# Optimization experiments

Hardware: AMD Instinct MI355X
Metric: run time of the kernel (lower is better)

The kernel has to match this reference:

```python
import jax, jax.numpy as jnp
import numpy as np

N_NODES = 50000
N_EDGES = 800000
IN_CH = 64
HID = 128


def setup_inputs() -> dict:
    key = jax.random.key(0)
    ks = jax.random.split(key, 10)
    x = jax.random.normal(ks[0], (N_NODES, IN_CH), dtype=jnp.float32)
    edge_index = jax.random.randint(ks[1], (2, N_EDGES), 0, N_NODES, dtype=jnp.int64)
    def lin(k, fan_in, fan_out):
        bound = 1.0 / np.sqrt(fan_in)
        kw, kb = jax.random.split(k)
        W = jax.random.uniform(kw, (fan_in, fan_out), minval=-bound, maxval=bound, dtype=jnp.float32)
        b = jax.random.uniform(kb, (fan_out,), minval=-bound, maxval=bound, dtype=jnp.float32)
        return W, b
    W1a, b1a = lin(ks[2], 2 * IN_CH, HID)
    W1b, b1b = lin(ks[3], HID, HID)
    W2a, b2a = lin(ks[4], 2 * HID, HID)
    W2b, b2b = lin(ks[5], HID, HID)
    return {"x": x, "edge_index": edge_index,
            "W1a": W1a, "b1a": b1a, "W1b": W1b, "b1b": b1b,
            "W2a": W2a, "b2a": b2a, "W2b": W2b, "b2b": b2b}


def _edge_conv(x, src, dst, Wa, ba, Wb, bb):
    # PyG EdgeConv: message = MLP([x_i, x_j - x_i]), aggr = max at target i (dst)
    xi = x[dst]                                   # [E, C] target feats
    xj = x[src]                                   # [E, C] source feats
    m = jnp.concatenate([xi, xj - xi], axis=-1)   # [E, 2C]
    m = jax.nn.relu(m @ Wa + ba) @ Wb + bb        # [E, H]
    agg = jax.ops.segment_max(m, dst, num_segments=N_NODES)
    # nodes with no incoming edge -> 0 (torch_scatter fill value)
    return jnp.where(jnp.isfinite(agg), agg, 0.0)


def reference(x, edge_index, W1a, b1a, W1b, b1b, W2a, b2a, W2b, b2b):
    src = edge_index[0]
    dst = edge_index[1]
    h = _edge_conv(x, src, dst, W1a, b1a, W1b, b1b)
    h = jax.nn.relu(h)
    h = _edge_conv(h, src, dst, W2a, b2a, W2b, b2b)
    return h
```

## Files before the change

kernel.cpp:

```cpp
#include <hip/hip_runtime.h>
#include <stdint.h>

#define N_NODES 50000
#define N_EDGES 800000
#define HID 128
#define NWG_E (N_EDGES / 128)
#define XQ (NWG_E / 8)
#define XR (NWG_E % 8)
#define SCAN_B 196

#define ENC_NEG_INF 0x007FFFFFu

typedef short short8 __attribute__((ext_vector_type(8)));
typedef float f32x4 __attribute__((ext_vector_type(4)));

__device__ __forceinline__ unsigned enc_f32(float f) {
    unsigned u = __float_as_uint(f);
    return (u & 0x80000000u) ? ~u : (u | 0x80000000u);
}
__device__ __forceinline__ float dec_f32(unsigned e) {
    unsigned u = (e & 0x80000000u) ? (e & 0x7FFFFFFFu) : ~e;
    return __uint_as_float(u);
}
__device__ __forceinline__ unsigned short f2bf(float f) {
    unsigned u = __float_as_uint(f);
    unsigned r = (u + 0x7fffu + ((u >> 16) & 1u)) >> 16;
    return (unsigned short)r;
}
__device__ __forceinline__ float bf2f(unsigned short h) {
    return __uint_as_float(((unsigned)h) << 16);
}
__device__ __forceinline__ float wcat_val(const float* __restrict__ W, int K, int k, int n) {
    return (n < 128) ? (W[k * 128 + n] - W[(k + K) * 128 + n]) : W[(k + K) * 128 + (n - 128)];
}

__global__ __launch_bounds__(256) void setup(
        const float* __restrict__ W1a, const float* __restrict__ W1b,
        const float* __restrict__ W2a, const float* __restrict__ W2b,
        unsigned short* __restrict__ Wg1, unsigned short* __restrict__ Wg2,
        unsigned short* __restrict__ WCg1, unsigned short* __restrict__ WCg2,
        unsigned* __restrict__ AGG1, unsigned* __restrict__ OUT,
        unsigned* __restrict__ count) {
    int bid = blockIdx.x, tid = threadIdx.x;
    const int NH = N_NODES * HID;

    if (bid < 128) {
        const float* Wb = (bid < 64) ? W1b : W2b;
        unsigned short* Wg = (bid < 64) ? Wg1 : Wg2;
        int idx = (bid & 63) * 256 + tid;
        int j = idx & 7, l = (idx >> 3) & 63, t = idx >> 9;
        int h = t >> 4, kt = (t >> 2) & 3, ntl = t & 3;
        int nt = 4 * h + ntl;
        int k = 32 * kt + 8 * (l >> 4) + j;
        int n = 16 * nt + (l & 15);
        Wg[idx] = f2bf(Wb[k * 128 + n]);
    } else if (bid < 192) {
        int idx = (bid - 128) * 256 + tid;
        int j = idx & 7, l = (idx >> 3) & 63, nt = (idx >> 9) & 15, kt = idx >> 13;
        int k = 32 * kt + 8 * (l >> 4) + j;
        int n = 16 * nt + (l & 15);
        float v = wcat_val(W1a, 64, k, n);
        unsigned short hi = f2bf(v);
        WCg1[idx] = hi;
        WCg1[64 * 256 + idx] = f2bf(v - bf2f(hi));
    } else if (bid < 320) {
        int idx = (bid - 192) * 256 + tid;
        int j = idx & 7, l = (idx >> 3) & 63, nt = (idx >> 9) & 15, kt = idx >> 13;
        int k = 32 * kt + 8 * (l >> 4) + j;
        int n = 16 * nt + (l & 15);
        float v = wcat_val(W2a, 128, k, n);
        unsigned short hi = f2bf(v);
        WCg2[idx] = hi;
        WCg2[128 * 256 + idx] = f2bf(v - bf2f(hi));
    }

    int total = 2 * NH + N_NODES;
    for (int i = bid * 256 + tid; i < total; i += gridDim.x * 256) {
        if (i < NH) AGG1[i] = ENC_NEG_INF;
        else if (i < 2 * NH) OUT[i - NH] = ENC_NEG_INF;
        else count[i - 2 * NH] = 0u;
    }
}

__global__ void out_decode(unsigned* __restrict__ p, const float* __restrict__ bias, int n) {
    int i = blockIdx.x * blockDim.x + threadIdx.x;
    int stride = gridDim.x * blockDim.x;
    for (; i < n; i += stride) {
        unsigned e = p[i];
        float f = (e == ENC_NEG_INF) ? 0.0f : dec_f32(e) + bias[i & 127];
        ((float*)p)[i] = f;
    }
}


__global__ void hist_dst(const int* __restrict__ dst, unsigned* __restrict__ count) {
    int i = blockIdx.x * blockDim.x + threadIdx.x;
    if (i < N_EDGES) atomicAdd(&count[dst[i]], 1u);
}

__global__ __launch_bounds__(256) void scan_p1(const unsigned* __restrict__ count,
                                               unsigned* __restrict__ bsum) {
    __shared__ unsigned s[256];
    int t = threadIdx.x;
    int i = blockIdx.x * 256 + t;
    s[t] = (i < N_NODES) ? count[i] : 0u;
    __syncthreads();
    for (int off = 128; off > 0; off >>= 1) {
        if (t < off) s[t] += s[t + off];
        __syncthreads();
    }
    if (t == 0) bsum[blockIdx.x] = s[0];
}

__global__ __launch_bounds__(256) void scan_p2(unsigned* __restrict__ bsum) {
    __shared__ unsigned s[256];
    int t = threadIdx.x;
    unsigned v = (t < SCAN_B) ? bsum[t] : 0u;
    s[t] = v;
    __syncthreads();
    for (int off = 1; off < 256; off <<= 1) {
        unsigned x = (t >= off) ? s[t - off] : 0u;
        __syncthreads();
        s[t] += x;
        __syncthreads();
    }
    if (t < SCAN_B) bsum[t] = s[t] - v;
}

__global__ __launch_bounds__(256) void scan_p3(const unsigned* __restrict__ count,
                                               const unsigned* __restrict__ bsum,
                                               unsigned* __restrict__ cursor) {
    __shared__ unsigned s[256];
    int t = threadIdx.x;
    int i = blockIdx.x * 256 + t;
    unsigned v = (i < N_NODES) ? count[i] : 0u;
    s[t] = v;
    __syncthreads();
    for (int off = 1; off < 256; off <<= 1) {
        unsigned x = (t >= off) ? s[t - off] : 0u;
        __syncthreads();
        s[t] += x;
        __syncthreads();
    }
    if (i < N_NODES) cursor[i] = bsum[blockIdx.x] + s[t] - v;
}

__global__ void scatter_edges(const int* __restrict__ src, const int* __restrict__ dst,
                              unsigned* __restrict__ cursor,
                              int* __restrict__ ssrc, int* __restrict__ sdst) {
    int i = blockIdx.x * blockDim.x + threadIdx.x;
    if (i < N_EDGES) {
        int d = dst[i];
        unsigned p = atomicAdd(&cursor[d], 1u);
        ssrc[p] = src[i];
        sdst[p] = d;
    }
}

template<int DEC, int KT>
__global__ __launch_bounds__(256, 2) void gemm_uv_mfma(
        const void* __restrict__ A_,
        const unsigned short* __restrict__ Wg,
        const float* __restrict__ bprev,
        const float* __restrict__ bu,
        unsigned short* __restrict__ C,
        int M) {
    __shared__ char lds[KT * 8192];
    const int K = 32 * KT;
    int tid = threadIdx.x;
    int bx = blockIdx.x, by = blockIdx.y;
    int r0 = bx * 128;
    int w = tid >> 6, l = tid & 63;
    int q = l >> 4, m = l & 15;

    short8 ahi[2][KT];
#pragma unroll
    for (int mt = 0; mt < 2; ++mt) {
        int row = r0 + 32 * w + 16 * mt + m;
        bool ok = row < M;
#pragma unroll
        for (int kt = 0; kt < KT; ++kt) {
            float av[8] = {0.f, 0.f, 0.f, 0.f, 0.f, 0.f, 0.f, 0.f};
            if (ok) {
                if (DEC) {
                    const unsigned* Ar = (const unsigned*)A_ + (size_t)row * K + 32 * kt + 8 * q;
                    uint4 x0 = *(const uint4*)Ar;
                    uint4 x1 = *(const uint4*)(Ar + 4);
                    float4 g0 = *(const float4*)&bprev[32 * kt + 8 * q];
                    float4 g1 = *(const float4*)&bprev[32 * kt + 8 * q + 4];
                    av[0] = fmaxf(dec_f32(x0.x) + g0.x, 0.f);
                    av[1] = fmaxf(dec_f32(x0.y) + g0.y, 0.f);
                    av[2] = fmaxf(dec_f32(x0.z) + g0.z, 0.f);
                    av[3] = fmaxf(dec_f32(x0.w) + g0.w, 0.f);
                    av[4] = fmaxf(dec_f32(x1.x) + g1.x, 0.f);
                    av[5] = fmaxf(dec_f32(x1.y) + g1.y, 0.f);
                    av[6] = fmaxf(dec_f32(x1.z) + g1.z, 0.f);
                    av[7] = fmaxf(dec_f32(x1.w) + g1.w, 0.f);
                } else {
                    const float* Ar = (const float*)A_ + (size_t)row * K + 32 * kt + 8 * q;
                    float4 f0 = *(const float4*)Ar;
                    float4 f1 = *(const float4*)(Ar + 4);
                    av[0] = f0.x; av[1] = f0.y; av[2] = f0.z; av[3] = f0.w;
                    av[4] = f1.x; av[5] = f1.y; av[6] = f1.z; av[7] = f1.w;
                }
            }
            short8 hi;
#pragma unroll
            for (int j = 0; j < 8; ++j) hi[j] = (short)f2bf(av[j]);
            ahi[mt][kt] = hi;
        }
    }

    f32x4 acc[2][8];
#pragma unroll
    for (int mt = 0; mt < 2; ++mt)
#pragma unroll
        for (int nt = 0; nt < 8; ++nt)
            acc[mt][nt] = (f32x4){0.f, 0.f, 0.f, 0.f};

    const short8* bfr = (const short8*)lds;

#pragma unroll
    for (int pl = 0; pl < 2; ++pl) {
        if (pl) __syncthreads();
        {
            const float4* s4 = (const float4*)Wg + (size_t)pl * (K * 32);
            float4* d4 = (float4*)lds;
#pragma unroll
            for (int it = 0; it < 2 * KT; ++it) {
                int f = 256 * it + tid;
                int tl = f >> 6, fin = f & 63;
                int tg = (tl >> 3) * 16 + 8 * by + (tl & 7);
                d4[f] = s4[tg * 64 + fin];
            }
        }
        __syncthreads();
#pragma unroll
        for (int nt = 0; nt < 8; ++nt)
#pragma unroll
            for (int kt = 0; kt < KT; ++kt) {
                short8 b = bfr[(kt * 8 + nt) * 64 + l];
                acc[0][nt] = __builtin_amdgcn_mfma_f32_16x16x32_bf16(ahi[0][kt], b, acc[0][nt], 0, 0, 0);
                acc[1][nt] = __builtin_amdgcn_mfma_f32_16x16x32_bf16(ahi[1][kt], b, acc[1][nt], 0, 0, 0);
            }
    }

#pragma unroll
    for (int nt = 0; nt < 8; ++nt) {
        float bias = (by == 0) ? bu[16 * nt + m] : 0.f;
#pragma unroll
        for (int mt = 0; mt < 2; ++mt) {
            int rowb = r0 + 32 * w + 16 * mt + 4 * q;
#pragma unroll
            for (int r = 0; r < 4; ++r) {
                int row = rowb + r;
                if (row < M)
                    C[(size_t)row * 256 + 128 * by + 16 * nt + m] = f2bf(acc[mt][nt][r] + bias);
            }
        }
    }
}

__global__ __launch_bounds__(256, 4) void edge_mlp_mfma(
        const unsigned short* __restrict__ UV,
        const unsigned short* __restrict__ Wg,
        const int* __restrict__ ssrc,
        const int* __restrict__ sdst,
        unsigned* __restrict__ AGG) {
    __shared__ char lds[17408];
    __shared__ int sdst_s[128];
    int tid = threadIdx.x;
    int orig = blockIdx.x;
    int xcd = orig & 7, ii = orig >> 3;
    int wg = (xcd < XR) ? xcd * (XQ + 1) + ii : XR * (XQ + 1) + (xcd - XR) * XQ + ii;
    int e0 = wg * 128;
    int w = tid >> 6, l = tid & 63;
    int q = l >> 4, m = l & 15;

    if (tid < 128) sdst_s[tid] = sdst[e0 + tid];

    short8 ahi[2][4];
    {
        int eA = e0 + 32 * w + m;
        int d0 = sdst[eA], s0 = ssrc[eA];
        int d1 = sdst[eA + 16], s1 = ssrc[eA + 16];
        const short8* Ud0 = (const short8*)&UV[(size_t)d0 * 256];
        const short8* Vs0 = (const short8*)&UV[(size_t)s0 * 256 + 128];
        const short8* Ud1 = (const short8*)&UV[(size_t)d1 * 256];
        const short8* Vs1 = (const short8*)&UV[(size_t)s1 * 256 + 128];
        short8 ub[2][4], vb[2][4];
#pragma unroll
        for (int kt = 0; kt < 4; ++kt) {
            ub[0][kt] = Ud0[4 * kt + q];
            vb[0][kt] = Vs0[4 * kt + q];
            ub[1][kt] = Ud1[4 * kt + q];
            vb[1][kt] = Vs1[4 * kt + q];
        }
#pragma unroll
        for (int mt = 0; mt < 2; ++mt)
#pragma unroll
            for (int kt = 0; kt < 4; ++kt) {
                short8 hi;
#pragma unroll
                for (int j = 0; j < 8; ++j) {
                    float t = bf2f((unsigned short)ub[mt][kt][j]) + bf2f((unsigned short)vb[mt][kt][j]);
                    hi[j] = (short)f2bf(fmaxf(t, 0.f));
                }
                ahi[mt][kt] = hi;
            }
    }

    const short8* bfr = (const short8*)lds;
    float* M2 = (float*)lds;
    f32x4 acc[2][4];

#pragma unroll
    for (int h = 0; h < 2; ++h) {
        __syncthreads();
        {
            const float4* s4 = (const float4*)Wg + h * 1024;
            float4* d4 = (float4*)lds;
#pragma unroll
            for (int i = 0; i < 4; ++i) d4[tid + 256 * i] = s4[tid + 256 * i];
        }
        __syncthreads();
#pragma unroll
        for (int mt = 0; mt < 2; ++mt)
#pragma unroll
            for (int ntl = 0; ntl < 4; ++ntl)
                acc[mt][ntl] = (f32x4){0.f, 0.f, 0.f, 0.f};
#pragma unroll
        for (int ntl = 0; ntl < 4; ++ntl)
#pragma unroll
            for (int kt = 0; kt < 4; ++kt) {
                short8 b = bfr[(kt * 4 + ntl) * 64 + l];
                acc[0][ntl] = __builtin_amdgcn_mfma_f32_16x16x32_bf16(ahi[0][kt], b, acc[0][ntl], 0, 0, 0);
                acc[1][ntl] = __builtin_amdgcn_mfma_f32_16x16x32_bf16(ahi[1][kt], b, acc[1][ntl], 0, 0, 0);
            }

#pragma unroll
        for (int cn = 0; cn < 2; ++cn) {
            __syncthreads();
#pragma unroll
            for (int nt2 = 0; nt2 < 2; ++nt2) {
                int ntl = 2 * cn + nt2;
#pragma unroll
                for (int mt = 0; mt < 2; ++mt)
#pragma unroll
                    for (int r = 0; r < 4; ++r)
                        M2[(32 * w + 16 * mt + 4 * q + r) * 34 + 16 * nt2 + m] = acc[mt][ntl][r];
            }
            __syncthreads();
            {
                int c = tid & 31, g = tid >> 5;
                int eb = 16 * g;
                int cur = sdst_s[eb];
                float mx = -3.402823466e38f;
                for (int e2 = eb; e2 < eb + 16; ++e2) {
                    int de = sdst_s[e2];
                    if (de != cur) {
                        atomicMax(&AGG[(size_t)cur * 128 + 64 * h + 32 * cn + c], enc_f32(mx));
                        cur = de;
                        mx = -3.402823466e38f;
                    }
                    mx = fmaxf(mx, M2[e2 * 34 + c]);
                }
                atomicMax(&AGG[(size_t)cur * 128 + 64 * h + 32 * cn + c], enc_f32(mx));
            }
        }
    }
}


extern "C" void kernel_launch(void* const* d_in, const int* in_sizes, int n_in,
                              void* d_out, int out_size, void* d_ws, size_t ws_size,
                              hipStream_t stream) {
    const float* x   = (const float*)d_in[0];
    const int*   ei  = (const int*)d_in[1];
    const float* W1a = (const float*)d_in[2];
    const float* b1a = (const float*)d_in[3];
    const float* W1b = (const float*)d_in[4];
    const float* b1b = (const float*)d_in[5];
    const float* W2a = (const float*)d_in[6];
    const float* b2a = (const float*)d_in[7];
    const float* W2b = (const float*)d_in[8];
    const float* b2b = (const float*)d_in[9];
    const int* src = ei;
    const int* dst = ei + N_EDGES;

    char* ws = (char*)d_ws;
    unsigned short* UV    = (unsigned short*)ws;
    unsigned*       AGG1  = (unsigned*)(ws + 25600000);
    int*            ssrc  = (int*)(ws + 51200000);
    int*            sdst  = (int*)(ws + 54400000);
    unsigned*       count = (unsigned*)(ws + 57600000);
    unsigned*       cursor= (unsigned*)(ws + 57800000);
    unsigned short* Wg1   = (unsigned short*)(ws + 58000000);
    unsigned short* Wg2   = (unsigned short*)(ws + 58065536);
    unsigned short* WCg1  = (unsigned short*)(ws + 58327680);
    unsigned short* WCg2  = (unsigned short*)(ws + 58393216);
    unsigned*       bsum  = (unsigned*)(ws + 58655744);

    const int NH = N_NODES * HID;

    setup<<<2048, 256, 0, stream>>>(W1a, W1b, W2a, W2b, Wg1, Wg2, WCg1, WCg2,
                                    AGG1, (unsigned*)d_out, count);

    hist_dst<<<3125, 256, 0, stream>>>(dst, count);
    scan_p1<<<SCAN_B, 256, 0, stream>>>(count, bsum);
    scan_p2<<<1, 256, 0, stream>>>(bsum);
    scan_p3<<<SCAN_B, 256, 0, stream>>>(count, bsum, cursor);
    scatter_edges<<<3125, 256, 0, stream>>>(src, dst, cursor, ssrc, sdst);

    gemm_uv_mfma<0, 2><<<dim3(391, 2), 256, 0, stream>>>(x, WCg1, nullptr, b1a, UV, N_NODES);
    edge_mlp_mfma<<<NWG_E, 256, 0, stream>>>(UV, Wg1, ssrc, sdst, AGG1);

    gemm_uv_mfma<1, 4><<<dim3(391, 2), 256, 0, stream>>>(AGG1, WCg2, b1b, b2a, UV, N_NODES);
    edge_mlp_mfma<<<NWG_E, 256, 0, stream>>>(UV, Wg2, ssrc, sdst, (unsigned*)d_out);
    out_decode<<<2048, 256, 0, stream>>>((unsigned*)d_out, b2b, NH);
}
```

Measured before the change: 314.9 us.

## Load full weight tile once and use per-wave LDS scratch to drop block barriers

The edge MLP kernel now stages both halves of the second-layer weights into LDS in one pass before the loop, instead of reloading per half behind two barriers. Each wave gets its own scratch region for the segment-max reduction, and destination indices are held in registers. This removes all block-level syncs inside the loop, and the weight load overlaps the bf16 relu conversion. The cost is more LDS per block (about 49KB), so launch bounds drop from 4 to 3 blocks per SIMD, which may lower occupancy.

```diff
diff --git a/kernel.cpp b/kernel.cpp
--- a/kernel.cpp
+++ b/kernel.cpp
@@ -261,14 +261,13 @@
     }
 }
 
-__global__ __launch_bounds__(256, 4) void edge_mlp_mfma(
+__global__ __launch_bounds__(256, 3) void edge_mlp_mfma(
         const unsigned short* __restrict__ UV,
         const unsigned short* __restrict__ Wg,
         const int* __restrict__ ssrc,
         const int* __restrict__ sdst,
         unsigned* __restrict__ AGG) {
-    __shared__ char lds[17408];
-    __shared__ int sdst_s[128];
+    __shared__ char lds[32768 + 4 * 4352];
     int tid = threadIdx.x;
     int orig = blockIdx.x;
     int xcd = orig & 7, ii = orig >> 3;
@@ -277,9 +276,7 @@
     int w = tid >> 6, l = tid & 63;
     int q = l >> 4, m = l & 15;
 
-    if (tid < 128) sdst_s[tid] = sdst[e0 + tid];
-
-    short8 ahi[2][4];
+    short8 ub[2][4], vb[2][4];
     {
         int eA = e0 + 32 * w + m;
         int d0 = sdst[eA], s0 = ssrc[eA];
@@ -288,7 +285,6 @@
         const short8* Vs0 = (const short8*)&UV[(size_t)s0 * 256 + 128];
         const short8* Ud1 = (const short8*)&UV[(size_t)d1 * 256];
         const short8* Vs1 = (const short8*)&UV[(size_t)s1 * 256 + 128];
-        short8 ub[2][4], vb[2][4];
 #pragma unroll
         for (int kt = 0; kt < 4; ++kt) {
             ub[0][kt] = Ud0[4 * kt + q];
@@ -296,34 +292,43 @@
             ub[1][kt] = Ud1[4 * kt + q];
             vb[1][kt] = Vs1[4 * kt + q];
         }
-#pragma unroll
-        for (int mt = 0; mt < 2; ++mt)
-#pragma unroll
-            for (int kt = 0; kt < 4; ++kt) {
-                short8 hi;
-#pragma unroll
-                for (int j = 0; j < 8; ++j) {
-                    float t = bf2f((unsigned short)ub[mt][kt][j]) + bf2f((unsigned short)vb[mt][kt][j]);
-                    hi[j] = (short)f2bf(fmaxf(t, 0.f));
-                }
-                ahi[mt][kt] = hi;
-            }
-    }
+    }
+
+    int4 dw[4];
+    {
+        const int4* dsrc = (const int4*)&sdst[e0 + 32 * w + 16 * (l >> 5)];
+        dw[0] = dsrc[0]; dw[1] = dsrc[1]; dw[2] = dsrc[2]; dw[3] = dsrc[3];
+    }
+
+    {
+        const float4* s4 = (const float4*)Wg;
+        float4* d4 = (float4*)lds;
+#pragma unroll
+        for (int i = 0; i < 8; ++i) d4[tid + 256 * i] = s4[tid + 256 * i];
+    }
+
+    short8 ahi[2][4];
+#pragma unroll
+    for (int mt = 0; mt < 2; ++mt)
+#pragma unroll
+        for (int kt = 0; kt < 4; ++kt) {
+            short8 hi;
+#pragma unroll
+            for (int j = 0; j < 8; ++j) {
+                float t = bf2f((unsigned short)ub[mt][kt][j]) + bf2f((unsigned short)vb[mt][kt][j]);
+                hi[j] = (short)f2bf(fmaxf(t, 0.f));
+            }
+            ahi[mt][kt] = hi;
+        }
+
+    __syncthreads();
 
     const short8* bfr = (const short8*)lds;
-    float* M2 = (float*)lds;
+    float* M2 = (float*)(lds + 32768 + w * 4352);
     f32x4 acc[2][4];
 
 #pragma unroll
     for (int h = 0; h < 2; ++h) {
-        __syncthreads();
-        {
-            const float4* s4 = (const float4*)Wg + h * 1024;
-            float4* d4 = (float4*)lds;
-#pragma unroll
-            for (int i = 0; i < 4; ++i) d4[tid + 256 * i] = s4[tid + 256 * i];
-        }
-        __syncthreads();
 #pragma unroll
         for (int mt = 0; mt < 2; ++mt)
 #pragma unroll
@@ -333,14 +338,13 @@
         for (int ntl = 0; ntl < 4; ++ntl)
 #pragma unroll
             for (int kt = 0; kt < 4; ++kt) {
-                short8 b = bfr[(kt * 4 + ntl) * 64 + l];
+                short8 b = bfr[(h * 16 + kt * 4 + ntl) * 64 + l];
                 acc[0][ntl] = __builtin_amdgcn_mfma_f32_16x16x32_bf16(ahi[0][kt], b, acc[0][ntl], 0, 0, 0);
                 acc[1][ntl] = __builtin_amdgcn_mfma_f32_16x16x32_bf16(ahi[1][kt], b, acc[1][ntl], 0, 0, 0);
             }
 
 #pragma unroll
         for (int cn = 0; cn < 2; ++cn) {
-            __syncthreads();
 #pragma unroll
             for (int nt2 = 0; nt2 < 2; ++nt2) {
                 int ntl = 2 * cn + nt2;
@@ -348,22 +352,22 @@
                 for (int mt = 0; mt < 2; ++mt)
 #pragma unroll
                     for (int r = 0; r < 4; ++r)
-                        M2[(32 * w + 16 * mt + 4 * q + r) * 34 + 16 * nt2 + m] = acc[mt][ntl][r];
-            }
-            __syncthreads();
+                        M2[(16 * mt + 4 * q + r) * 34 + 16 * nt2 + m] = acc[mt][ntl][r];
+            }
             {
-                int c = tid & 31, g = tid >> 5;
-                int eb = 16 * g;
-                int cur = sdst_s[eb];
+                int c = l & 31;
+                const int* dwp = (const int*)dw;
+                int cur = dwp[0];
                 float mx = -3.402823466e38f;
-                for (int e2 = eb; e2 < eb + 16; ++e2) {
-                    int de = sdst_s[e2];
+#pragma unroll
+                for (int i = 0; i < 16; ++i) {
+                    int de = dwp[i];
                     if (de != cur) {
                         atomicMax(&AGG[(size_t)cur * 128 + 64 * h + 32 * cn + c], enc_f32(mx));
                         cur = de;
                         mx = -3.402823466e38f;
                     }
-                    mx = fmaxf(mx, M2[e2 * 34 + c]);
+                    mx = fmaxf(mx, M2[(16 * (l >> 5) + i) * 34 + c]);
                 }
                 atomicMax(&AGG[(size_t)cur * 128 + 64 * h + 32 * cn + c], enc_f32(mx));
             }
```

Result: no change. 309.1 us (-1.8%).
